# Kernel optimization log

Hardware: AMD Instinct MI355X
Metric: run time of the kernel (lower is better)

The kernel has to match this reference:

```python
import jax, jax.numpy as jnp
import numpy as np

N = 100000   # nodes
E = 3200000  # edges (before self-loops)
G = 256      # graphs in batch
IN_DIM, HID, OUT3 = 25, 64, 32


def setup_inputs() -> dict:
    key = jax.random.key(0)
    ks = jax.random.split(key, 13)
    def w(k, shape, fan_in):
        return jax.random.normal(k, shape, jnp.float32) * (1.0 / np.sqrt(fan_in))
    return {
        "x": jax.random.normal(ks[0], (N, IN_DIM), jnp.float32),
        "edge_index": jax.random.randint(ks[1], (2, E), 0, N, dtype=jnp.int32),
        "batch": jnp.sort(jax.random.randint(ks[2], (N,), 0, G, dtype=jnp.int32)),
        "W1": w(ks[3], (IN_DIM, HID), IN_DIM), "b1": jnp.zeros((HID,), jnp.float32),
        "W2": w(ks[4], (HID, HID), HID),       "b2": jnp.zeros((HID,), jnp.float32),
        "W3": w(ks[5], (HID, OUT3), HID),      "b3": jnp.zeros((OUT3,), jnp.float32),
        "Wh1": w(ks[6], (OUT3, 32), OUT3),     "bh1": jnp.zeros((32,), jnp.float32),
        "Wh2": w(ks[7], (32, 1), 32),          "bh2": jnp.zeros((1,), jnp.float32),
    }


def _gcn_layer(x, W, b, src, dst, num_nodes):
    # GCNConv: h = W^T x; out_i = sum_j norm_ij * h_j (+ self-loop), norm = d_i^-1/2 d_j^-1/2
    h = x @ W  # [N, F_out]
    ones = jnp.ones(src.shape[0], h.dtype)
    deg = jax.ops.segment_sum(ones, dst, num_segments=num_nodes)  # includes self-loops -> >= 1
    dinv = jax.lax.rsqrt(jnp.maximum(deg, 1.0))
    norm = dinv[src] * dinv[dst]                       # [E+N]
    msgs = h[src] * norm[:, None]                       # gather + scale
    out = jax.ops.segment_sum(msgs, dst, num_segments=num_nodes)  # scatter-add
    return out + b


def reference(x, edge_index, batch, W1, b1, W2, b2, W3, b3, Wh1, bh1, Wh2, bh2):
    n = x.shape[0]
    loops = jnp.arange(n, dtype=edge_index.dtype)
    src = jnp.concatenate([edge_index[0], loops])  # add self-loops
    dst = jnp.concatenate([edge_index[1], loops])

    h = jax.nn.relu(_gcn_layer(x, W1, b1, src, dst, n))
    h = jax.nn.relu(_gcn_layer(h, W2, b2, src, dst, n))
    h = jax.nn.relu(_gcn_layer(h, W3, b3, src, dst, n))

    # global mean pool over graphs
    counts = jax.ops.segment_sum(jnp.ones(n, h.dtype), batch, num_segments=G)
    g = jax.ops.segment_sum(h, batch, num_segments=G) / jnp.maximum(counts, 1.0)[:, None]

    y = jax.nn.relu(g @ Wh1 + bh1) @ Wh2 + bh2  # [G, 1]
    return y.squeeze(-1)
```

## Files before the change

### kernel.cpp

```cpp
#include <hip/hip_runtime.h>
#include <hip/hip_fp16.h>


#define IN_DIM 25
#define HID 64
#define OUT3 32
#define BK_LOG 6
#define BK_NODES 64
#define CB_LOG 8
#define NCB 512
#define EPB1 8192
#define BCAP2 10240
#define RNG_LOG 14
#define NR 8
#define NKEY2 2048

__global__ __launch_bounds__(256) void bucket_hist(const int* __restrict__ dst,
                                                   int* __restrict__ bhist, int nE) {
    __shared__ int h[NCB];
    for (int i = threadIdx.x; i < NCB; i += 256) h[i] = 0;
    __syncthreads();
    int e0 = blockIdx.x * 8192;
    int cnt = min(8192, nE - e0);
    for (int i = threadIdx.x; i < cnt; i += 256)
        atomicAdd(&h[(unsigned)dst[e0 + i] >> CB_LOG], 1);
    __syncthreads();
    for (int i = threadIdx.x; i < NCB; i += 256)
        if (h[i]) atomicAdd(&bhist[i], h[i]);
}

__global__ __launch_bounds__(256) void bucket_scan(const int* __restrict__ bhist,
                                                   int* __restrict__ bbase,
                                                   int* __restrict__ cursor,
                                                   int nb, int nE) {
    __shared__ int s4[256];
    int t = threadIdx.x;
    int v[2]; int sum = 0;
#pragma unroll
    for (int j = 0; j < 2; ++j) {
        int b = 2 * t + j;
        v[j] = (b < nb) ? bhist[b] : 0;
        sum += v[j];
    }
    s4[t] = sum;
    __syncthreads();
    for (int off = 1; off < 256; off <<= 1) {
        int mine = s4[t];
        int add = (t >= off) ? s4[t - off] : 0;
        __syncthreads();
        s4[t] = mine + add;
        __syncthreads();
    }
    int run = s4[t] - sum;
#pragma unroll
    for (int j = 0; j < 2; ++j) {
        int b = 2 * t + j;
        if (b < nb) { bbase[b] = run; cursor[b] = run; }
        run += v[j];
    }
    if (t == 0) bbase[nb] = nE;
}

__global__ __launch_bounds__(256) void partition_kernel(
        const int* __restrict__ src, const int* __restrict__ dst,
        int* __restrict__ cursor, unsigned int* __restrict__ ebuf, int nE) {
    __shared__ int lh[NCB];
    __shared__ int lrun[NCB];
    int t = threadIdx.x;
    int e0 = blockIdx.x * EPB1;
    int cnt = min(EPB1, nE - e0);
    for (int i = t; i < NCB; i += 256) lh[i] = 0;
    __syncthreads();
    for (int i = t; i < cnt; i += 256)
        atomicAdd(&lh[(unsigned)dst[e0 + i] >> CB_LOG], 1);
    __syncthreads();
    for (int b = t; b < NCB; b += 256) {
        int v = lh[b];
        lh[b] = 0;
        if (v > 0) lrun[b] = atomicAdd(&cursor[b], v);
    }
    __syncthreads();
    for (int i = t; i < cnt; i += 256) {
        int d = dst[e0 + i];
        int s = src[e0 + i];
        int cb = (unsigned)d >> CB_LOG;
        int lp = atomicAdd(&lh[cb], 1);
        unsigned int w = ((unsigned)(d & 255) << 17) | (unsigned)s;
        ebuf[lrun[cb] + lp] = w;
    }
}

__global__ __launch_bounds__(256) void coarse_sort_kernel(
        unsigned int* __restrict__ ebuf, const int* __restrict__ bbase,
        float* __restrict__ dinv, int* __restrict__ gp64, int* __restrict__ gp32,
        int nN) {
    int cb = blockIdx.x;
    int node_lo = cb << CB_LOG;
    int base = bbase[cb];
    int cnt = bbase[cb + 1] - base;
    if (cnt > BCAP2) cnt = BCAP2;
    __shared__ unsigned int in[BCAP2];
    __shared__ int h[NKEY2];
    __shared__ int sc[NKEY2 + 1];
    __shared__ int swp[256];
    int t = threadIdx.x;
    for (int i = t; i < cnt; i += 256) in[i] = ebuf[base + i];
    for (int i = t; i < NKEY2; i += 256) h[i] = 0;
    __syncthreads();
    for (int i = t; i < cnt; i += 256) {
        unsigned int w = in[i];
        int kk = (int)(((w >> 23) & 3u) << 9) | (int)(((w >> RNG_LOG) & 7u) << 6)
               | (int)((w >> 17) & 63u);
        atomicAdd(&h[kk], 1);
    }
    __syncthreads();
    int v[8]; int sum = 0;
#pragma unroll
    for (int j = 0; j < 8; ++j) { v[j] = h[8 * t + j]; sum += v[j]; }
    swp[t] = sum;
    __syncthreads();
    for (int off = 1; off < 256; off <<= 1) {
        int mine = swp[t];
        int add = (t >= off) ? swp[t - off] : 0;
        __syncthreads();
        swp[t] = mine + add;
        __syncthreads();
    }
    int run = swp[t] - sum;
#pragma unroll
    for (int j = 0; j < 8; ++j) { sc[8 * t + j] = run; run += v[j]; }
    if (t == 255) sc[NKEY2] = run;
    __syncthreads();
    {
        int fb = t >> 6, idx = t & 63;
        gp64[(cb * 4 + fb) * 65 + idx] = base + sc[(fb << 9) | (idx << 3)];
    }
    if (t < 4) gp64[(cb * 4 + t) * 65 + 64] = base + sc[(t + 1) << 9];
    for (int i = t; i < 512; i += 256) {
        int fb = i >> 7, idx = i & 127;
        gp32[(cb * 4 + fb) * 129 + idx] = base + sc[(fb << 9) | (idx << 2)];
    }
    if (t < 4) gp32[(cb * 4 + t) * 129 + 128] = base + sc[(t + 1) << 9];
    {
        int node = node_lo + t;
        if (node < nN) {
            int fb = t >> 6, dl = t & 63;
            int deg = 0;
#pragma unroll
            for (int r = 0; r < NR; ++r) {
                int k = (fb << 9) | (r << 6) | dl;
                deg += sc[k + 1] - sc[k];
            }
            dinv[node] = rsqrtf((float)deg + 1.0f);
        }
    }
    for (int i = t; i < NKEY2; i += 256) h[i] = 0;
    __syncthreads();
    for (int i = t; i < cnt; i += 256) {
        unsigned int w = in[i];
        int kk = (int)(((w >> 23) & 3u) << 9) | (int)(((w >> RNG_LOG) & 7u) << 6)
               | (int)((w >> 17) & 63u);
        int lp = atomicAdd(&h[kk], 1);
        ebuf[base + sc[kk] + lp] = w & 0x7FFFFFu;
    }
}

__global__ void padx_kernel(const float* __restrict__ x, const float* __restrict__ dinv,
                            __half* __restrict__ xp, int n) {
    int i = blockIdx.x * 256 + threadIdx.x;
    if (i < n * 16) {
        int node = i >> 4, c2 = (i & 15) * 2;
        float s = dinv[node];
        float v0 = (c2     < IN_DIM) ? x[(size_t)node * IN_DIM + c2    ] * s : 0.f;
        float v1 = (c2 + 1 < IN_DIM) ? x[(size_t)node * IN_DIM + c2 + 1] * s : 0.f;
        *(__half2*)&xp[(size_t)node * 32 + c2] = __floats2half2_rn(v0, v1);
    }
}

__global__ void padw_kernel(const float* __restrict__ W1, float* __restrict__ W1p) {
    int i = blockIdx.x * 256 + threadIdx.x;
    if (i < 32 * HID) {
        int r = i >> 6, c = i & 63;
        W1p[i] = (r < IN_DIM) ? W1[r * HID + c] : 0.f;
    }
}

template<int INF, int OUTF, bool ACT, bool SCALE>
__global__ __launch_bounds__(256) void gemm_kernel(
        const float* __restrict__ in, const float* __restrict__ W,
        const float* __restrict__ bias, const float* __restrict__ dinv,
        void* __restrict__ out, int n) {
    constexpr int TPN = OUTF / 4;
    constexpr int NPB = 256 / TPN;
    constexpr int LDK = INF + 4;
    __shared__ float sW[INF * OUTF];
    __shared__ float sIn[NPB][LDK];
    for (int i = threadIdx.x; i < INF * OUTF; i += 256) sW[i] = W[i];
    int node0 = blockIdx.x * NPB;
    for (int i = threadIdx.x; i < NPB * INF; i += 256) {
        int ln = i / INF, k = i % INF;
        int node = node0 + ln;
        sIn[ln][k] = (node < n) ? in[(size_t)node * INF + k] : 0.f;
    }
    __syncthreads();
    int g   = threadIdx.x / TPN;
    int of0 = (threadIdx.x % TPN) * 4;
    int node = node0 + g;
    float4 acc = make_float4(0.f, 0.f, 0.f, 0.f);
#pragma unroll
    for (int k = 0; k < INF; ++k) {
        float aj = sIn[g][k];
        const float4 wv = *(const float4*)&sW[k * OUTF + of0];
        acc.x += aj * wv.x; acc.y += aj * wv.y;
        acc.z += aj * wv.z; acc.w += aj * wv.w;
    }
    if (ACT) {
        const float4 bv = *(const float4*)&bias[of0];
        acc.x = fmaxf(acc.x + bv.x, 0.f);
        acc.y = fmaxf(acc.y + bv.y, 0.f);
        acc.z = fmaxf(acc.z + bv.z, 0.f);
        acc.w = fmaxf(acc.w + bv.w, 0.f);
    }
    if (node < n) {
        if (SCALE) {
            float s = dinv[node];
            union { __half2 h[2]; uint2 u; } pk;
            pk.h[0] = __floats2half2_rn(acc.x * s, acc.y * s);
            pk.h[1] = __floats2half2_rn(acc.z * s, acc.w * s);
            *(uint2*)((__half*)out + (size_t)node * OUTF + of0) = pk.u;
        } else {
            *(float4*)((float*)out + (size_t)node * OUTF + of0) = acc;
        }
    }
}

template<int F, bool ACT>
__global__ __launch_bounds__(256, 6) void gatherp_kernel(
        const __half* __restrict__ hp, const float* __restrict__ dinv,
        const int* __restrict__ gp, const unsigned int* __restrict__ eb,
        const float* __restrict__ bias, float* __restrict__ agg, int n) {
    constexpr int LPN = F / 2;
    constexpr int G   = 256 / LPN;
    constexpr int GPB = NR * G + 1;
    __shared__ float acc[(BK_NODES + 1) * F];
    int b = blockIdx.x, t = threadIdx.x;
    int node_lo = b << BK_LOG;
    for (int i = t; i < BK_NODES * LPN; i += 256) {
        int ln = i / LPN, c2 = (i % LPN) * 2;
        int node = node_lo + ln;
        float2 v = make_float2(0.f, 0.f);
        if (node < n)
            v = __half22float2(*(const __half2*)&hp[(size_t)node * F + c2]);
        acc[ln * F + c2] = v.x;
        acc[ln * F + c2 + 1] = v.y;
    }
    __syncthreads();
    int g  = t / LPN;
    int c2 = (t % LPN) * 2;
    float ax = 0.f, ay = 0.f;
    int cur = BK_NODES;
    for (int r = 0; r < NR; ++r) {
        int e  = gp[b * GPB + r * G + g];
        int e1 = gp[b * GPB + r * G + g + 1];
        for (; e + 8 <= e1; e += 8) {
            unsigned int w[8];
#pragma unroll
            for (int u = 0; u < 8; ++u) w[u] = eb[e + u];
            float2 v[8];
#pragma unroll
            for (int u = 0; u < 8; ++u)
                v[u] = __half22float2(
                    *(const __half2*)&hp[(size_t)(w[u] & 0x1FFFFu) * F + c2]);
#pragma unroll
            for (int u = 0; u < 8; ++u) {
                int dl = (int)(w[u] >> 17);
                if (dl != cur) {
                    acc[cur * F + c2]     += ax;
                    acc[cur * F + c2 + 1] += ay;
                    ax = 0.f; ay = 0.f; cur = dl;
                }
                ax += v[u].x; ay += v[u].y;
            }
        }
        for (; e < e1; ++e) {
            unsigned int w = eb[e];
            float2 v = __half22float2(
                *(const __half2*)&hp[(size_t)(w & 0x1FFFFu) * F + c2]);
            int dl = (int)(w >> 17);
            if (dl != cur) {
                acc[cur * F + c2]     += ax;
                acc[cur * F + c2 + 1] += ay;
                ax = 0.f; ay = 0.f; cur = dl;
            }
            ax += v.x; ay += v.y;
        }
        acc[cur * F + c2]     += ax;
        acc[cur * F + c2 + 1] += ay;
        ax = 0.f; ay = 0.f; cur = BK_NODES;
        __syncthreads();
    }
    for (int i = t; i < BK_NODES * LPN; i += 256) {
        int ln = i / LPN, cc = (i % LPN) * 2;
        int node = node_lo + ln;
        if (node < n) {
            float s = dinv[node];
            float rx = acc[ln * F + cc] * s;
            float ry = acc[ln * F + cc + 1] * s;
            if (ACT) {
                rx = fmaxf(rx + bias[cc], 0.f);
                ry = fmaxf(ry + bias[cc + 1], 0.f);
            }
            union { float2 f; unsigned long long u; } o;
            o.f = make_float2(rx, ry);
            __builtin_nontemporal_store(o.u,
                (unsigned long long*)&agg[(size_t)node * F + cc]);
        }
    }
}

__global__ __launch_bounds__(256) void pool_kernel(
        const float* __restrict__ h3, const int* __restrict__ batch,
        int n, float* __restrict__ pool) {
    int g = blockIdx.x;
    int lo = 0, hi = n;
    while (lo < hi) { int m = (lo + hi) >> 1; if (batch[m] < g) lo = m + 1; else hi = m; }
    int s = lo;
    hi = n;
    while (lo < hi) { int m = (lo + hi) >> 1; if (batch[m] < g + 1) lo = m + 1; else hi = m; }
    int e = lo;
    constexpr int F = OUT3;
    int ln = threadIdx.x / F;
    int f  = threadIdx.x % F;
    float acc = 0.f;
    for (int i = s + ln; i < e; i += 8)
        acc += h3[(size_t)i * F + f];
    __shared__ float red[8][F];
    red[ln][f] = acc;
    __syncthreads();
    if (ln == 0) {
        float t = 0.f;
#pragma unroll
        for (int j = 0; j < 8; ++j) t += red[j][f];
        float cnt = (float)((e - s) > 0 ? (e - s) : 1);
        pool[g * F + f] = t / cnt;
    }
}

__global__ __launch_bounds__(256) void head_kernel(
        const float* __restrict__ pool, const float* __restrict__ Wh1,
        const float* __restrict__ bh1, const float* __restrict__ Wh2,
        const float* __restrict__ bh2, float* __restrict__ out) {
    __shared__ float sW1[32 * 32];
    __shared__ float sb1[32];
    __shared__ float sW2[32];
    int t = threadIdx.x;
    for (int i = t; i < 1024; i += 256) sW1[i] = Wh1[i];
    if (t < 32) { sb1[t] = bh1[t]; sW2[t] = Wh2[t]; }
    __syncthreads();
    int g = t;
    float y = bh2[0];
    const float* p = &pool[g * 32];
#pragma unroll 4
    for (int j = 0; j < 32; ++j) {
        float a = sb1[j];
#pragma unroll
        for (int k = 0; k < 32; ++k) a += p[k] * sW1[k * 32 + j];
        y += fmaxf(a, 0.f) * sW2[j];
    }
    out[g] = y;
}

extern "C" void kernel_launch(void* const* d_in, const int* in_sizes, int n_in,
                              void* d_out, int out_size, void* d_ws, size_t ws_size,
                              hipStream_t stream) {
    const float* x    = (const float*)d_in[0];
    const int*   ei   = (const int*)  d_in[1];
    const int*   batch= (const int*)  d_in[2];
    const float* W1   = (const float*)d_in[3];
    const float* b1   = (const float*)d_in[4];
    const float* W2   = (const float*)d_in[5];
    const float* b2   = (const float*)d_in[6];
    const float* W3   = (const float*)d_in[7];
    const float* b3   = (const float*)d_in[8];
    const float* Wh1  = (const float*)d_in[9];
    const float* bh1  = (const float*)d_in[10];
    const float* Wh2  = (const float*)d_in[11];
    const float* bh2  = (const float*)d_in[12];
    float* out = (float*)d_out;

    const int N = in_sizes[0] / IN_DIM;
    const int E = in_sizes[1] / 2;
    const int* src = ei;
    const int* dst = ei + E;
    const int NB = (N + BK_NODES - 1) >> BK_LOG;

    char* base = (char*)d_ws;
    unsigned int* ebuf = (unsigned int*)base;       base += (size_t)E * 4;
    int*   bhist   = (int*)base;                    base += (size_t)NCB * 4;
    int*   bbase   = (int*)base;                    base += (size_t)(NCB + 1) * 4;
    int*   cursor  = (int*)base;                    base += (size_t)NCB * 4;
    int*   gp64    = (int*)base;                    base += (size_t)(NCB * 4) * 65 * 4;
    int*   gp32    = (int*)base;                    base += (size_t)(NCB * 4) * 129 * 4;
    float* dinv    = (float*)base;                  base += (size_t)N * 4;
    float* W1p     = (float*)base;                  base += (size_t)32 * HID * 4;
    float* bufA    = (float*)base;                  base += (size_t)N * HID * 4;
    float* bufB    = (float*)base;                  base += (size_t)N * HID * 4;
    float* pool    = (float*)base;

    hipMemsetAsync(bhist, 0, (size_t)NCB * sizeof(int), stream);
    bucket_hist<<<(E + 8191) / 8192, 256, 0, stream>>>(dst, bhist, E);
    bucket_scan<<<1, 256, 0, stream>>>(bhist, bbase, cursor, NCB, E);
    partition_kernel<<<(E + EPB1 - 1) / EPB1, 256, 0, stream>>>(src, dst, cursor, ebuf, E);
    coarse_sort_kernel<<<NCB, 256, 0, stream>>>(ebuf, bbase, dinv, gp64, gp32, N);

    padx_kernel<<<((size_t)N * 16 + 255) / 256, 256, 0, stream>>>(x, dinv, (__half*)bufB, N);
    padw_kernel<<<(32 * HID + 255) / 256, 256, 0, stream>>>(W1, W1p);
    gatherp_kernel<32, false><<<NB, 256, 0, stream>>>((const __half*)bufB, dinv, gp32, ebuf, nullptr, bufA, N);
    gemm_kernel<32, HID, true, false><<<(N + 15) / 16, 256, 0, stream>>>(bufA, W1p, b1, nullptr, bufB, N);

    gemm_kernel<HID, HID, false, true><<<(N + 15) / 16, 256, 0, stream>>>(bufB, W2, nullptr, dinv, bufA, N);
    gatherp_kernel<64, true><<<NB, 256, 0, stream>>>((const __half*)bufA, dinv, gp64, ebuf, b2, bufB, N);

    gemm_kernel<HID, OUT3, false, true><<<(N + 31) / 32, 256, 0, stream>>>(bufB, W3, nullptr, dinv, bufA, N);
    gatherp_kernel<32, true><<<NB, 256, 0, stream>>>((const __half*)bufA, dinv, gp32, ebuf, b3, bufB, N);

    pool_kernel<<<256, 256, 0, stream>>>(bufB, batch, N, pool);
    head_kernel<<<1, 256, 0, stream>>>(pool, Wh1, bh1, Wh2, bh2, out);
}
```

Before: 458.3 us.

## Assign one wavefront per edge segment with lane-per-feature gather

Reworks the gather kernel so each 64-lane wavefront walks a contiguous edge segment, with edge words broadcast through readfirstlane and each lane handling one half-precision feature. Previously groups of F/2 lanes each took a sub-segment and loaded half2 pairs. The segment pointer table becomes a single 33-entry-per-block layout shared across all three layers, replacing the separate 64- and 32-feature tables. The goal is scalar edge-index loads and less per-lane index traffic. In exchange, F=32 leaves half the lanes idle and the loads become narrower 2-byte accesses, and each wave has fewer parallel segments, which may expose load latency.

```diff
diff --git a/kernel.cpp b/kernel.cpp
--- a/kernel.cpp
+++ b/kernel.cpp
@@ -14,6 +14,7 @@
 #define RNG_LOG 14
 #define NR 8
 #define NKEY2 2048
+#define GPB 33
 
 __global__ __launch_bounds__(256) void bucket_hist(const int* __restrict__ dst,
                                                    int* __restrict__ bhist, int nE) {
@@ -92,8 +93,7 @@
 
 __global__ __launch_bounds__(256) void coarse_sort_kernel(
         unsigned int* __restrict__ ebuf, const int* __restrict__ bbase,
-        float* __restrict__ dinv, int* __restrict__ gp64, int* __restrict__ gp32,
-        int nN) {
+        float* __restrict__ dinv, int* __restrict__ gp, int nN) {
     int cb = blockIdx.x;
     int node_lo = cb << CB_LOG;
     int base = bbase[cb];
@@ -131,16 +131,12 @@
     for (int j = 0; j < 8; ++j) { sc[8 * t + j] = run; run += v[j]; }
     if (t == 255) sc[NKEY2] = run;
     __syncthreads();
-    {
-        int fb = t >> 6, idx = t & 63;
-        gp64[(cb * 4 + fb) * 65 + idx] = base + sc[(fb << 9) | (idx << 3)];
-    }
-    if (t < 4) gp64[(cb * 4 + t) * 65 + 64] = base + sc[(t + 1) << 9];
-    for (int i = t; i < 512; i += 256) {
-        int fb = i >> 7, idx = i & 127;
-        gp32[(cb * 4 + fb) * 129 + idx] = base + sc[(fb << 9) | (idx << 2)];
-    }
-    if (t < 4) gp32[(cb * 4 + t) * 129 + 128] = base + sc[(t + 1) << 9];
+    if (t < 128) {
+        int fb = t >> 5, idx = t & 31;
+        int r = idx >> 2, g = idx & 3;
+        gp[(cb * 4 + fb) * GPB + idx] = base + sc[(fb << 9) | (r << 6) | (g << 4)];
+    }
+    if (t < 4) gp[(cb * 4 + t) * GPB + 32] = base + sc[(t + 1) << 9];
     {
         int node = node_lo + t;
         if (node < nN) {
@@ -235,13 +231,11 @@
 }
 
 template<int F, bool ACT>
-__global__ __launch_bounds__(256, 6) void gatherp_kernel(
+__global__ __launch_bounds__(256, 6) void gatherw_kernel(
         const __half* __restrict__ hp, const float* __restrict__ dinv,
         const int* __restrict__ gp, const unsigned int* __restrict__ eb,
         const float* __restrict__ bias, float* __restrict__ agg, int n) {
     constexpr int LPN = F / 2;
-    constexpr int G   = 256 / LPN;
-    constexpr int GPB = NR * G + 1;
     __shared__ float acc[(BK_NODES + 1) * F];
     int b = blockIdx.x, t = threadIdx.x;
     int node_lo = b << BK_LOG;
@@ -255,48 +249,46 @@
         acc[ln * F + c2 + 1] = v.y;
     }
     __syncthreads();
-    int g  = t / LPN;
-    int c2 = (t % LPN) * 2;
-    float ax = 0.f, ay = 0.f;
+    int wv   = __builtin_amdgcn_readfirstlane(t >> 6);
+    int lane = t & 63;
+    int lf   = lane & (F - 1);
+    bool own = (F == 64) || (lane < F);
+    float a = 0.f;
     int cur = BK_NODES;
     for (int r = 0; r < NR; ++r) {
-        int e  = gp[b * GPB + r * G + g];
-        int e1 = gp[b * GPB + r * G + g + 1];
+        int e  = __builtin_amdgcn_readfirstlane(gp[b * GPB + r * 4 + wv]);
+        int e1 = __builtin_amdgcn_readfirstlane(gp[b * GPB + r * 4 + wv + 1]);
         for (; e + 8 <= e1; e += 8) {
             unsigned int w[8];
 #pragma unroll
-            for (int u = 0; u < 8; ++u) w[u] = eb[e + u];
-            float2 v[8];
-#pragma unroll
             for (int u = 0; u < 8; ++u)
-                v[u] = __half22float2(
-                    *(const __half2*)&hp[(size_t)(w[u] & 0x1FFFFu) * F + c2]);
+                w[u] = (unsigned)__builtin_amdgcn_readfirstlane((int)eb[e + u]);
+            float v[8];
+#pragma unroll
+            for (int u = 0; u < 8; ++u)
+                v[u] = __half2float(hp[(size_t)(w[u] & 0x1FFFFu) * F + lf]);
 #pragma unroll
             for (int u = 0; u < 8; ++u) {
                 int dl = (int)(w[u] >> 17);
                 if (dl != cur) {
-                    acc[cur * F + c2]     += ax;
-                    acc[cur * F + c2 + 1] += ay;
-                    ax = 0.f; ay = 0.f; cur = dl;
+                    if (own) acc[cur * F + lf] += a;
+                    a = 0.f; cur = dl;
                 }
-                ax += v[u].x; ay += v[u].y;
+                a += v[u];
             }
         }
         for (; e < e1; ++e) {
-            unsigned int w = eb[e];
-            float2 v = __half22float2(
-                *(const __half2*)&hp[(size_t)(w & 0x1FFFFu) * F + c2]);
+            unsigned int w = (unsigned)__builtin_amdgcn_readfirstlane((int)eb[e]);
+            float v = __half2float(hp[(size_t)(w & 0x1FFFFu) * F + lf]);
             int dl = (int)(w >> 17);
             if (dl != cur) {
-                acc[cur * F + c2]     += ax;
-                acc[cur * F + c2 + 1] += ay;
-                ax = 0.f; ay = 0.f; cur = dl;
+                if (own) acc[cur * F + lf] += a;
+                a = 0.f; cur = dl;
             }
-            ax += v.x; ay += v.y;
+            a += v;
         }
-        acc[cur * F + c2]     += ax;
-        acc[cur * F + c2 + 1] += ay;
-        ax = 0.f; ay = 0.f; cur = BK_NODES;
+        if (own) acc[cur * F + lf] += a;
+        a = 0.f; cur = BK_NODES;
         __syncthreads();
     }
     for (int i = t; i < BK_NODES * LPN; i += 256) {
@@ -399,8 +391,7 @@
     int*   bhist   = (int*)base;                    base += (size_t)NCB * 4;
     int*   bbase   = (int*)base;                    base += (size_t)(NCB + 1) * 4;
     int*   cursor  = (int*)base;                    base += (size_t)NCB * 4;
-    int*   gp64    = (int*)base;                    base += (size_t)(NCB * 4) * 65 * 4;
-    int*   gp32    = (int*)base;                    base += (size_t)(NCB * 4) * 129 * 4;
+    int*   gp      = (int*)base;                    base += (size_t)(NCB * 4) * GPB * 4;
     float* dinv    = (float*)base;                  base += (size_t)N * 4;
     float* W1p     = (float*)base;                  base += (size_t)32 * HID * 4;
     float* bufA    = (float*)base;                  base += (size_t)N * HID * 4;
@@ -411,18 +402,18 @@
     bucket_hist<<<(E + 8191) / 8192, 256, 0, stream>>>(dst, bhist, E);
     bucket_scan<<<1, 256, 0, stream>>>(bhist, bbase, cursor, NCB, E);
     partition_kernel<<<(E + EPB1 - 1) / EPB1, 256, 0, stream>>>(src, dst, cursor, ebuf, E);
-    coarse_sort_kernel<<<NCB, 256, 0, stream>>>(ebuf, bbase, dinv, gp64, gp32, N);
+    coarse_sort_kernel<<<NCB, 256, 0, stream>>>(ebuf, bbase, dinv, gp, N);
 
     padx_kernel<<<((size_t)N * 16 + 255) / 256, 256, 0, stream>>>(x, dinv, (__half*)bufB, N);
     padw_kernel<<<(32 * HID + 255) / 256, 256, 0, stream>>>(W1, W1p);
-    gatherp_kernel<32, false><<<NB, 256, 0, stream>>>((const __half*)bufB, dinv, gp32, ebuf, nullptr, bufA, N);
+    gatherw_kernel<32, false><<<NB, 256, 0, stream>>>((const __half*)bufB, dinv, gp, ebuf, nullptr, bufA, N);
     gemm_kernel<32, HID, true, false><<<(N + 15) / 16, 256, 0, stream>>>(bufA, W1p, b1, nullptr, bufB, N);
 
     gemm_kernel<HID, HID, false, true><<<(N + 15) / 16, 256, 0, stream>>>(bufB, W2, nullptr, dinv, bufA, N);
-    gatherp_kernel<64, true><<<NB, 256, 0, stream>>>((const __half*)bufA, dinv, gp64, ebuf, b2, bufB, N);
+    gatherw_kernel<64, true><<<NB, 256, 0, stream>>>((const __half*)bufA, dinv, gp, ebuf, b2, bufB, N);
 
     gemm_kernel<HID, OUT3, false, true><<<(N + 31) / 32, 256, 0, stream>>>(bufB, W3, nullptr, dinv, bufA, N);
-    gatherp_kernel<32, true><<<NB, 256, 0, stream>>>((const __half*)bufA, dinv, gp32, ebuf, b3, bufB, N);
+    gatherw_kernel<32, true><<<NB, 256, 0, stream>>>((const __half*)bufA, dinv, gp, ebuf, b3, bufB, N);
 
     pool_kernel<<<256, 256, 0, stream>>>(bufB, batch, N, pool);
     head_kernel<<<1, 256, 0, stream>>>(pool, Wh1, bh1, Wh2, bh2, out);
```

Result: slower. 535.1 us (+16.8%).
